# Performance work log

Hardware: AMD Instinct MI355X
Metric: run time of the kernel (lower is better)

The kernel has to match this reference:

```python
import jax, jax.numpy as jnp
import numpy as np

EPS = 1e-5

def rmsnorm(x, w):
    return x * jax.lax.rsqrt(jnp.mean(x * x, axis=-1, keepdims=True) + EPS) * w

def setup_inputs() -> dict:
    key = jax.random.key(0)
    ks = jax.random.split(key, 10)
    b, d, n, k, r, l = 64, 256, 16, 4, 16, 256
    inp = {}
    inp['x_1'] = jax.random.normal(ks[0], (b, d), jnp.float32)
    inp['x_2'] = jax.random.normal(ks[1], (b, d), jnp.float32)
    inp['norm_w'] = jnp.ones((d,), jnp.float32)
    inp['conv_w'] = jax.random.normal(ks[2], (d, 1, k), jnp.float32) * 0.2
    inp['conv_b'] = jax.random.normal(ks[3], (d,), jnp.float32) * 0.02
    inp['in_w'] = jax.random.normal(ks[4], (2 * d, d), jnp.float32) * 0.02
    inp['xproj_w'] = jax.random.normal(ks[5], (r + 2 * n, d), jnp.float32) * 0.02
    inp['dt_w'] = jax.random.normal(ks[6], (d, r), jnp.float32) * 0.02
    inp['dt_b'] = jax.random.normal(ks[7], (d,), jnp.float32) * 0.02
    inp['out_w'] = jax.random.normal(ks[8], (d, d), jnp.float32) * 0.02
    # A = repeat(arange(1, n+1), 'n -> d n'); A_log = log(A)
    inp['A_log'] = jnp.tile(jnp.log(jnp.arange(1, n + 1, dtype=jnp.float32)), (d, 1))
    inp['D'] = jnp.ones((d,), jnp.float32)
    inp['l'] = l
    return inp

def _dwconv(x, conv_w, conv_b, l):
    # x: (b, l, d); depthwise causal-ish conv with padding k-1 on both sides, truncate to l
    d = x.shape[-1]
    k = conv_w.shape[-1]
    xt = x.transpose(0, 2, 1)  # (b, d, l)
    out = jax.lax.conv_general_dilated(
        xt, conv_w, window_strides=(1,), padding=[(k - 1, k - 1)],
        dimension_numbers=('NCH', 'OIH', 'NCH'), feature_group_count=d)
    out = out[:, :, :l] + conv_b[None, :, None]
    return out.transpose(0, 2, 1)  # (b, l, d)

def reference(x_1, x_2, norm_w, conv_w, conv_b, in_w, xproj_w, dt_w, dt_b, out_w, A_log, D, l):
    b, d = x_1.shape
    n = A_log.shape[1]
    r = dt_w.shape[1]
    # RMSNorm then broadcast along sequence
    x1 = jnp.broadcast_to(rmsnorm(x_1, norm_w)[:, None, :], (b, l, d))
    x2 = jnp.broadcast_to(rmsnorm(x_2, norm_w)[:, None, :], (b, l, d))
    # in_proj (no bias), split into x and res
    xr1 = x1 @ in_w.T
    x1c, res1 = xr1[..., :d], xr1[..., d:]
    xr2 = x2 @ in_w.T
    x2c, _ = xr2[..., :d], xr2[..., d:]
    # depthwise conv + silu
    x1s = jax.nn.silu(_dwconv(x1c, conv_w, conv_b, l))
    x2s = jax.nn.silu(_dwconv(x2c, conv_w, conv_b, l))
    # ssm: delta/B/C from x2s, scanned input u = x1s
    A = -jnp.exp(A_log)  # (d, n)
    xdbl = x2s @ xproj_w.T  # (b, l, r + 2n)
    delta, B, C = xdbl[..., :r], xdbl[..., r:r + n], xdbl[..., r + n:]
    delta = jax.nn.softplus(delta @ dt_w.T + dt_b)  # (b, l, d)
    deltaA = jnp.exp(jnp.einsum('bld,dn->bldn', delta, A))  # (b, l, d, n)
    dBu = (delta * x1s)[..., None] * B[:, :, None, :]  # (b, l, d, n)
    def step(h, inputs):
        dA_i, dBu_i, C_i = inputs  # (b,d,n), (b,d,n), (b,n)
        h = dA_i * h + dBu_i
        y = jnp.einsum('bdn,bn->bd', h, C_i)
        return h, y
    h0 = jnp.zeros((b, d, n), x1s.dtype)
    _, ys = jax.lax.scan(step, h0, (deltaA.transpose(1, 0, 2, 3),
                                     dBu.transpose(1, 0, 2, 3),
                                     C.transpose(1, 0, 2)))
    y = ys.transpose(1, 0, 2) + x1s * D  # (b, l, d)
    y = y * jax.nn.silu(res1)
    out = rmsnorm(y @ out_w.T, norm_w)
    return out[:, -1, :]
```

## Files before the change

kernel.cpp:

```cpp
#include <hip/hip_runtime.h>
#include <math.h>

#define D 256
#define N 16
#define R 16

#define WS_X1C  0
#define WS_RES1 16384
#define WS_X2C  32768

__device__ __forceinline__ float silu_f(float x) { return x / (1.0f + expf(-x)); }
__device__ __forceinline__ float softplus_f(float x) {
    return fmaxf(x, 0.0f) + log1pf(expf(-fabsf(x)));
}

__global__ __launch_bounds__(256) void k_inw(
    const float* __restrict__ x1_in, const float* __restrict__ x2_in,
    const float* __restrict__ norm_w, const float* __restrict__ in_w,
    float* __restrict__ ws)
{
    __shared__ float s_n[D];
    __shared__ float s_red[4];
    const int t  = threadIdx.x;
    const int g0 = blockIdx.x * 64;
    const int b  = g0 / 768;
    const int o0 = g0 % 768;
    const bool use2 = (o0 >= 512);

    const float* __restrict__ xrow = (use2 ? x2_in : x1_in) + (size_t)b * D;
    const float v = xrow[t];
    float p = v * v;
    #pragma unroll
    for (int off = 32; off >= 1; off >>= 1) p += __shfl_down(p, off, 64);
    if ((t & 63) == 0) s_red[t >> 6] = p;
    __syncthreads();
    const float ss = s_red[0] + s_red[1] + s_red[2] + s_red[3];
    s_n[t] = v * rsqrtf(ss * (1.0f / D) + 1e-5f) * norm_w[t];
    __syncthreads();

    const int o   = o0 + (t >> 2);
    const int q   = t & 3;
    const int row = (o >= 512) ? (o - 512) : o;
    const float* __restrict__ wr = in_w + (size_t)row * D;
    float acc = 0.0f;
    #pragma unroll
    for (int k = 0; k < 16; ++k) {
        const int e = q * 4 + 16 * k;
        const float4 w4 = *(const float4*)(wr + e);
        const float4 n4 = *(const float4*)(s_n + e);
        acc += w4.x*n4.x + w4.y*n4.y + w4.z*n4.z + w4.w*n4.w;
    }
    acc += __shfl_xor(acc, 1, 64);
    acc += __shfl_xor(acc, 2, 64);
    if (q == 0) {
        const int jj = o & 255;
        float* dst = (o < 256) ? (ws + WS_X1C)
                   : (o < 512) ? (ws + WS_RES1)
                               : (ws + WS_X2C);
        dst[b * D + jj] = acc;
    }
}

__global__ __launch_bounds__(1024) void k_fused(
    const float* __restrict__ conv_w, const float* __restrict__ conv_b,
    const float* __restrict__ xproj_w, const float* __restrict__ dt_w,
    const float* __restrict__ dt_b, const float* __restrict__ A_log,
    const float* __restrict__ Dp, const int* __restrict__ l_ptr,
    const float* __restrict__ out_w, const float* __restrict__ norm_w,
    const float* __restrict__ ws, float* __restrict__ out)
{
    __shared__ float s_x2s[4][D];
    __shared__ float s_xdbl[4][48];
    __shared__ float s_y[D];
    __shared__ float s_z[D];
    __shared__ float s_red[16];
    const int b = blockIdx.x;
    const int t = threadIdx.x;
    const int l = *l_ptr;

    float x1s[4];
    float res1 = 0.0f;
    if (t < D) {
        const float x1c = ws[WS_X1C + b * D + t];
        const float x2c = ws[WS_X2C + b * D + t];
        res1 = ws[WS_RES1 + b * D + t];
        const float4 cw = *(const float4*)(conv_w + 4 * t);
        const float cb  = conv_b[t];
        float ksum[4];
        ksum[0] = cw.w;
        ksum[1] = cw.z + cw.w;
        ksum[2] = cw.y + cw.z + cw.w;
        ksum[3] = cw.x + cw.y + cw.z + cw.w;
        #pragma unroll
        for (int tc = 0; tc < 4; ++tc) {
            x1s[tc] = silu_f(ksum[tc] * x1c + cb);
            s_x2s[tc][t] = silu_f(ksum[tc] * x2c + cb);
        }
    }
    __syncthreads();

    const int dotid = t >> 2;
    const int q     = t & 3;
    if (t < 768) {
        const int tc = dotid / 48;
        const int o  = dotid % 48;
        const float* __restrict__ pr = xproj_w + (size_t)o * D;
        const float* __restrict__ xs = s_x2s[tc];
        float acc = 0.0f;
        #pragma unroll
        for (int k = 0; k < 16; ++k) {
            const int e = q * 4 + 16 * k;
            const float4 p4 = *(const float4*)(pr + e);
            const float4 x4 = *(const float4*)(xs + e);
            acc += p4.x*x4.x + p4.y*x4.y + p4.z*x4.z + p4.w*x4.w;
        }
        acc += __shfl_xor(acc, 1, 64);
        acc += __shfl_xor(acc, 2, 64);
        if (q == 0) s_xdbl[tc][o] = acc;
    }
    __syncthreads();

    if (t < D) {
        const int j = t;
        const float* __restrict__ dtrow = dt_w + (size_t)j * R;
        float dtr[R];
        #pragma unroll
        for (int qq = 0; qq < R; ++qq) dtr[qq] = dtrow[qq];
        const float dtb = dt_b[j];
        float delta[4];
        #pragma unroll
        for (int tc = 0; tc < 4; ++tc) {
            float acc = 0.0f;
            #pragma unroll
            for (int qq = 0; qq < R; ++qq) acc += s_xdbl[tc][qq] * dtr[qq];
            delta[tc] = softplus_f(acc + dtb);
        }
        const float* __restrict__ arow = A_log + (size_t)j * N;
        float Aa[N];
        #pragma unroll
        for (int n = 0; n < N; ++n) Aa[n] = -expf(arow[n]);
        float h[N];
        #pragma unroll
        for (int n = 0; n < N; ++n) h[n] = 0.0f;
        const int nexp = (l < 3) ? l : 3;
        for (int tt = 0; tt < nexp; ++tt) {
            const float dl = delta[tt];
            const float du = dl * x1s[tt];
            #pragma unroll
            for (int n = 0; n < N; ++n) {
                const float dA = expf(dl * Aa[n]);
                h[n] = dA * h[n] + du * s_xdbl[tt][16 + n];
            }
        }
        if (l > 3) {
            const float dl = delta[3];
            const float du = dl * x1s[3];
            const float steps = (float)(l - 3);
            #pragma unroll
            for (int n = 0; n < N; ++n) {
                const float z   = dl * Aa[n];
                const float em1 = expm1f(z);
                const float emN = expm1f(steps * z);
                const float ratio = (em1 != 0.0f) ? (emN / em1) : steps;
                const float pw = emN + 1.0f;
                h[n] = pw * h[n] + du * s_xdbl[3][16 + n] * ratio;
            }
        }
        const int fc = ((l - 1) < 3) ? (l - 1) : 3;
        float y = 0.0f;
        #pragma unroll
        for (int n = 0; n < N; ++n) y += h[n] * s_xdbl[fc][32 + n];
        y += x1s[fc] * Dp[j];
        y *= silu_f(res1);
        s_y[j] = y;
    }
    __syncthreads();

    {
        const float* __restrict__ orow = out_w + (size_t)dotid * D;
        float acc = 0.0f;
        #pragma unroll
        for (int k = 0; k < 16; ++k) {
            const int e = q * 4 + 16 * k;
            const float4 w4 = *(const float4*)(orow + e);
            const float4 y4 = *(const float4*)(s_y + e);
            acc += w4.x*y4.x + w4.y*y4.y + w4.z*y4.z + w4.w*y4.w;
        }
        acc += __shfl_xor(acc, 1, 64);
        acc += __shfl_xor(acc, 2, 64);
        if (q == 0) s_z[dotid] = acc;
    }
    __syncthreads();

    const float zz = (t < D) ? s_z[t] : 0.0f;
    float p = zz * zz;
    #pragma unroll
    for (int off = 32; off >= 1; off >>= 1) p += __shfl_down(p, off, 64);
    if ((t & 63) == 0) s_red[t >> 6] = p;
    __syncthreads();
    if (t < D) {
        const float ss = s_red[0] + s_red[1] + s_red[2] + s_red[3];
        out[b * D + t] = zz * rsqrtf(ss * (1.0f / D) + 1e-5f) * norm_w[t];
    }
}

extern "C" void kernel_launch(void* const* d_in, const int* in_sizes, int n_in,
                              void* d_out, int out_size, void* d_ws, size_t ws_size,
                              hipStream_t stream) {
    const float* x1      = (const float*)d_in[0];
    const float* x2      = (const float*)d_in[1];
    const float* norm_w  = (const float*)d_in[2];
    const float* conv_w  = (const float*)d_in[3];
    const float* conv_b  = (const float*)d_in[4];
    const float* in_w    = (const float*)d_in[5];
    const float* xproj_w = (const float*)d_in[6];
    const float* dt_w    = (const float*)d_in[7];
    const float* dt_b    = (const float*)d_in[8];
    const float* out_w   = (const float*)d_in[9];
    const float* A_log   = (const float*)d_in[10];
    const float* Dp      = (const float*)d_in[11];
    const int*   l_ptr   = (const int*)d_in[12];
    float* out = (float*)d_out;
    float* ws  = (float*)d_ws;

    const int batch = in_sizes[0] / D;

    k_inw<<<dim3(batch * 12), dim3(256), 0, stream>>>(x1, x2, norm_w, in_w, ws);
    k_fused<<<dim3(batch), dim3(1024), 0, stream>>>(conv_w, conv_b, xproj_w,
                                                    dt_w, dt_b, A_log, Dp, l_ptr,
                                                    out_w, norm_w, ws, out);
}
```

Before: 95.42 us.

## Merge two kernels into one cooperative kernel with grid sync

Replaces the in-projection kernel and the fused per-batch kernel with a single cooperative launch of 256-thread blocks. A grid-wide sync separates the in_proj phase from the per-batch SSM phase, which avoids a second kernel launch. The later stages use 256 threads instead of 1024, so the remaining dot products are looped over fewer threads. In exchange it pays for the grid barrier, has three quarters of the blocks sit idle after the sync, and gives each block less parallelism for the xproj and out_proj work.

```diff
diff --git a/kernel.cpp b/kernel.cpp
--- a/kernel.cpp
+++ b/kernel.cpp
@@ -1,5 +1,8 @@
 #include <hip/hip_runtime.h>
+#include <hip/hip_cooperative_groups.h>
 #include <math.h>
+
+namespace cg = cooperative_groups;
 
 #define D 256
 #define N 16
@@ -14,73 +17,84 @@
     return fmaxf(x, 0.0f) + log1pf(expf(-fabsf(x)));
 }
 
-__global__ __launch_bounds__(256) void k_inw(
+__global__ __launch_bounds__(256) void k_mamba_all(
     const float* __restrict__ x1_in, const float* __restrict__ x2_in,
-    const float* __restrict__ norm_w, const float* __restrict__ in_w,
-    float* __restrict__ ws)
+    const float* __restrict__ norm_w, const float* __restrict__ conv_w,
+    const float* __restrict__ conv_b, const float* __restrict__ in_w,
+    const float* __restrict__ xproj_w, const float* __restrict__ dt_w,
+    const float* __restrict__ dt_b, const float* __restrict__ out_w,
+    const float* __restrict__ A_log, const float* __restrict__ Dp,
+    const int* __restrict__ l_ptr, float* __restrict__ ws,
+    float* __restrict__ out)
 {
-    __shared__ float s_n[D];
-    __shared__ float s_red[4];
-    const int t  = threadIdx.x;
-    const int g0 = blockIdx.x * 64;
-    const int b  = g0 / 768;
-    const int o0 = g0 % 768;
-    const bool use2 = (o0 >= 512);
-
-    const float* __restrict__ xrow = (use2 ? x2_in : x1_in) + (size_t)b * D;
-    const float v = xrow[t];
-    float p = v * v;
-    #pragma unroll
-    for (int off = 32; off >= 1; off >>= 1) p += __shfl_down(p, off, 64);
-    if ((t & 63) == 0) s_red[t >> 6] = p;
-    __syncthreads();
-    const float ss = s_red[0] + s_red[1] + s_red[2] + s_red[3];
-    s_n[t] = v * rsqrtf(ss * (1.0f / D) + 1e-5f) * norm_w[t];
-    __syncthreads();
-
-    const int o   = o0 + (t >> 2);
-    const int q   = t & 3;
-    const int row = (o >= 512) ? (o - 512) : o;
-    const float* __restrict__ wr = in_w + (size_t)row * D;
-    float acc = 0.0f;
-    #pragma unroll
-    for (int k = 0; k < 16; ++k) {
-        const int e = q * 4 + 16 * k;
-        const float4 w4 = *(const float4*)(wr + e);
-        const float4 n4 = *(const float4*)(s_n + e);
-        acc += w4.x*n4.x + w4.y*n4.y + w4.z*n4.z + w4.w*n4.w;
-    }
-    acc += __shfl_xor(acc, 1, 64);
-    acc += __shfl_xor(acc, 2, 64);
-    if (q == 0) {
-        const int jj = o & 255;
-        float* dst = (o < 256) ? (ws + WS_X1C)
-                   : (o < 512) ? (ws + WS_RES1)
-                               : (ws + WS_X2C);
-        dst[b * D + jj] = acc;
-    }
-}
-
-__global__ __launch_bounds__(1024) void k_fused(
-    const float* __restrict__ conv_w, const float* __restrict__ conv_b,
-    const float* __restrict__ xproj_w, const float* __restrict__ dt_w,
-    const float* __restrict__ dt_b, const float* __restrict__ A_log,
-    const float* __restrict__ Dp, const int* __restrict__ l_ptr,
-    const float* __restrict__ out_w, const float* __restrict__ norm_w,
-    const float* __restrict__ ws, float* __restrict__ out)
-{
+    __shared__ float s_n1[D];
+    __shared__ float s_n2[D];
     __shared__ float s_x2s[4][D];
     __shared__ float s_xdbl[4][48];
     __shared__ float s_y[D];
     __shared__ float s_z[D];
-    __shared__ float s_red[16];
-    const int b = blockIdx.x;
+    __shared__ float s_red[8];
+
     const int t = threadIdx.x;
+    const int g = blockIdx.x;
     const int l = *l_ptr;
 
+    {
+        const int b  = g >> 2;
+        const int qb = g & 3;
+        const float v1 = x1_in[b * D + t];
+        const float v2 = x2_in[b * D + t];
+        float p1 = v1 * v1, p2 = v2 * v2;
+        #pragma unroll
+        for (int off = 32; off >= 1; off >>= 1) {
+            p1 += __shfl_down(p1, off, 64);
+            p2 += __shfl_down(p2, off, 64);
+        }
+        if ((t & 63) == 0) { s_red[t >> 6] = p1; s_red[4 + (t >> 6)] = p2; }
+        __syncthreads();
+        const float ss1 = s_red[0] + s_red[1] + s_red[2] + s_red[3];
+        const float ss2 = s_red[4] + s_red[5] + s_red[6] + s_red[7];
+        const float wn = norm_w[t];
+        s_n1[t] = v1 * rsqrtf(ss1 * (1.0f / D) + 1e-5f) * wn;
+        s_n2[t] = v2 * rsqrtf(ss2 * (1.0f / D) + 1e-5f) * wn;
+        __syncthreads();
+
+        const int q = t & 3;
+        for (int it = 0; it < 3; ++it) {
+            const int o   = qb * 192 + it * 64 + (t >> 2);
+            const int row = (o >= 512) ? (o - 512) : o;
+            const float* __restrict__ wr = in_w + (size_t)row * D;
+            const float* __restrict__ xs = (o >= 512) ? s_n2 : s_n1;
+            float acc = 0.0f;
+            #pragma unroll
+            for (int k = 0; k < 16; ++k) {
+                const int e = q * 4 + 16 * k;
+                const float4 w4 = *(const float4*)(wr + e);
+                const float4 n4 = *(const float4*)(xs + e);
+                acc += w4.x*n4.x + w4.y*n4.y + w4.z*n4.z + w4.w*n4.w;
+            }
+            acc += __shfl_xor(acc, 1, 64);
+            acc += __shfl_xor(acc, 2, 64);
+            if (q == 0) {
+                const int jj = o & 255;
+                float* dst = (o < 256) ? (ws + WS_X1C)
+                           : (o < 512) ? (ws + WS_RES1)
+                                       : (ws + WS_X2C);
+                dst[b * D + jj] = acc;
+            }
+        }
+    }
+
+    __threadfence();
+    cg::this_grid().sync();
+
+    const int nbatch = gridDim.x >> 2;
+    if (g >= nbatch) return;
+    const int b = g;
+
     float x1s[4];
-    float res1 = 0.0f;
-    if (t < D) {
+    float res1;
+    {
         const float x1c = ws[WS_X1C + b * D + t];
         const float x2c = ws[WS_X2C + b * D + t];
         res1 = ws[WS_RES1 + b * D + t];
@@ -99,28 +113,30 @@
     }
     __syncthreads();
 
-    const int dotid = t >> 2;
-    const int q     = t & 3;
-    if (t < 768) {
-        const int tc = dotid / 48;
-        const int o  = dotid % 48;
-        const float* __restrict__ pr = xproj_w + (size_t)o * D;
-        const float* __restrict__ xs = s_x2s[tc];
-        float acc = 0.0f;
-        #pragma unroll
-        for (int k = 0; k < 16; ++k) {
-            const int e = q * 4 + 16 * k;
-            const float4 p4 = *(const float4*)(pr + e);
-            const float4 x4 = *(const float4*)(xs + e);
-            acc += p4.x*x4.x + p4.y*x4.y + p4.z*x4.z + p4.w*x4.w;
-        }
-        acc += __shfl_xor(acc, 1, 64);
-        acc += __shfl_xor(acc, 2, 64);
-        if (q == 0) s_xdbl[tc][o] = acc;
-    }
-    __syncthreads();
-
-    if (t < D) {
+    {
+        const int q = t & 3;
+        for (int it = 0; it < 3; ++it) {
+            const int dotid = it * 64 + (t >> 2);
+            const int tc = dotid / 48;
+            const int o  = dotid % 48;
+            const float* __restrict__ pr = xproj_w + (size_t)o * D;
+            const float* __restrict__ xs = s_x2s[tc];
+            float acc = 0.0f;
+            #pragma unroll
+            for (int k = 0; k < 16; ++k) {
+                const int e = q * 4 + 16 * k;
+                const float4 p4 = *(const float4*)(pr + e);
+                const float4 x4 = *(const float4*)(xs + e);
+                acc += p4.x*x4.x + p4.y*x4.y + p4.z*x4.z + p4.w*x4.w;
+            }
+            acc += __shfl_xor(acc, 1, 64);
+            acc += __shfl_xor(acc, 2, 64);
+            if (q == 0) s_xdbl[tc][o] = acc;
+        }
+    }
+    __syncthreads();
+
+    {
         const int j = t;
         const float* __restrict__ dtrow = dt_w + (size_t)j * R;
         float dtr[R];
@@ -177,28 +193,32 @@
     __syncthreads();
 
     {
-        const float* __restrict__ orow = out_w + (size_t)dotid * D;
-        float acc = 0.0f;
-        #pragma unroll
-        for (int k = 0; k < 16; ++k) {
-            const int e = q * 4 + 16 * k;
-            const float4 w4 = *(const float4*)(orow + e);
-            const float4 y4 = *(const float4*)(s_y + e);
-            acc += w4.x*y4.x + w4.y*y4.y + w4.z*y4.z + w4.w*y4.w;
-        }
-        acc += __shfl_xor(acc, 1, 64);
-        acc += __shfl_xor(acc, 2, 64);
-        if (q == 0) s_z[dotid] = acc;
-    }
-    __syncthreads();
-
-    const float zz = (t < D) ? s_z[t] : 0.0f;
-    float p = zz * zz;
-    #pragma unroll
-    for (int off = 32; off >= 1; off >>= 1) p += __shfl_down(p, off, 64);
-    if ((t & 63) == 0) s_red[t >> 6] = p;
-    __syncthreads();
-    if (t < D) {
+        const int q = t & 3;
+        for (int it = 0; it < 4; ++it) {
+            const int dotid = it * 64 + (t >> 2);
+            const float* __restrict__ orow = out_w + (size_t)dotid * D;
+            float acc = 0.0f;
+            #pragma unroll
+            for (int k = 0; k < 16; ++k) {
+                const int e = q * 4 + 16 * k;
+                const float4 w4 = *(const float4*)(orow + e);
+                const float4 y4 = *(const float4*)(s_y + e);
+                acc += w4.x*y4.x + w4.y*y4.y + w4.z*y4.z + w4.w*y4.w;
+            }
+            acc += __shfl_xor(acc, 1, 64);
+            acc += __shfl_xor(acc, 2, 64);
+            if (q == 0) s_z[dotid] = acc;
+        }
+    }
+    __syncthreads();
+
+    {
+        const float zz = s_z[t];
+        float p = zz * zz;
+        #pragma unroll
+        for (int off = 32; off >= 1; off >>= 1) p += __shfl_down(p, off, 64);
+        if ((t & 63) == 0) s_red[t >> 6] = p;
+        __syncthreads();
         const float ss = s_red[0] + s_red[1] + s_red[2] + s_red[3];
         out[b * D + t] = zz * rsqrtf(ss * (1.0f / D) + 1e-5f) * norm_w[t];
     }
@@ -225,8 +245,11 @@
 
     const int batch = in_sizes[0] / D;
 
-    k_inw<<<dim3(batch * 12), dim3(256), 0, stream>>>(x1, x2, norm_w, in_w, ws);
-    k_fused<<<dim3(batch), dim3(1024), 0, stream>>>(conv_w, conv_b, xproj_w,
-                                                    dt_w, dt_b, A_log, Dp, l_ptr,
-                                                    out_w, norm_w, ws, out);
+    void* args[] = {
+        (void*)&x1, (void*)&x2, (void*)&norm_w, (void*)&conv_w, (void*)&conv_b,
+        (void*)&in_w, (void*)&xproj_w, (void*)&dt_w, (void*)&dt_b, (void*)&out_w,
+        (void*)&A_log, (void*)&Dp, (void*)&l_ptr, (void*)&ws, (void*)&out
+    };
+    hipLaunchCooperativeKernel((const void*)k_mamba_all,
+                               dim3(batch * 4), dim3(256), args, 0, stream);
 }
```

Measured after the change: 166.3 us. +74.3%, slower.
